# Kernel optimization log

Measured on AMD Instinct MI355X. Metric: run time of the kernel, lower is better.

## Reference

```python
import jax, jax.numpy as jnp
import numpy as np

EMBED_DIM = 256
MIN_SCALE = 0.5
BASE = 100.0
NDIM = 3
EPS = 1e-5


def basis_norm(psi, w):
    # w: [B, N] float weights; reduce over token dim (-2)
    norm_sq = jnp.sum(w[..., None] * (psi * psi), axis=-2, keepdims=True)
    return psi / jnp.sqrt(norm_sq + EPS)


def rotary(f, coords, lift):
    # lift: [D//2, 3]; phase: [B, N, D//2]
    phase = coords @ lift.T
    c, s = jnp.cos(phase), jnp.sin(phase)
    f1, f2 = jnp.split(f, 2, axis=-1)
    return jnp.concatenate([f1 * c - f2 * s, f1 * s + f2 * c], axis=-1)


def setup_inputs() -> dict:
    key = jax.random.key(0)
    ks = jax.random.split(key, 12)
    B, N, D = 4, 8192, EMBED_DIM
    phi = jax.random.normal(ks[0], (B, N, D), dtype=jnp.float32)
    coords = jax.random.normal(ks[1], (B, N, NDIM), dtype=jnp.float32)
    weights = jax.random.uniform(ks[2], (B, N), dtype=jnp.float32)
    scale = 1.0 / np.sqrt(D)
    Wq = jax.random.normal(ks[3], (D, D), dtype=jnp.float32) * scale
    bq = jnp.zeros((D,), dtype=jnp.float32)
    Wk = jax.random.normal(ks[4], (D, D), dtype=jnp.float32) * scale
    bk = jax.random.normal(ks[5], (D,), dtype=jnp.float32) * 0.01
    Wv = jax.random.normal(ks[6], (D, D), dtype=jnp.float32) * scale
    bv = jax.random.normal(ks[7], (D,), dtype=jnp.float32) * 0.01
    Wo = jax.random.normal(ks[8], (D, D), dtype=jnp.float32) * scale
    bo = jnp.zeros((D,), dtype=jnp.float32)
    # rotary lift init: k_norms * random unit vecs
    half = D // 2
    scales = BASE ** (-2.0 * np.arange(half) / D)
    k_norms = (2.0 * np.pi / MIN_SCALE) * scales  # [half]
    u = np.asarray(jax.random.normal(ks[9], (half, NDIM)))
    u = u / np.linalg.norm(u, axis=-1, keepdims=True)
    lift = jnp.asarray(k_norms[:, None] * u, dtype=jnp.float32)  # [half, 3]
    return {"phi": phi, "coords": coords, "weights": weights,
            "Wq": Wq, "bq": bq, "Wk": Wk, "bk": bk, "Wv": Wv, "bv": bv,
            "Wo": Wo, "bo": bo, "lift": lift}


def reference(phi, coords, weights, Wq, bq, Wk, bk, Wv, bv, Wo, bo, lift):
    q = phi @ Wq.T + bq
    k = basis_norm(phi @ Wk.T + bk, weights)
    v = basis_norm(phi @ Wv.T + bv, weights)
    q = rotary(q, coords, lift)
    k = rotary(k, coords, lift)
    k = k * weights[..., None]  # float-weights branch
    kv = jnp.einsum('bnd,bne->bde', k, v)   # [B, D, D]
    out = jnp.einsum('bnd,bde->bne', q, kv)  # [B, N, D]
    return out @ Wo.T + bo
```

## Files before the change

### kernel.cpp

```cpp
#include <hip/hip_runtime.h>
#include <hip/hip_bf16.h>
#include <stdint.h>

#define DEV __device__ __forceinline__

typedef short short8 __attribute__((ext_vector_type(8)));
typedef float floatx4 __attribute__((ext_vector_type(4)));

constexpr int D = 256;
constexpr int NTOK = 8192;
constexpr int MTOT = 4 * NTOK;

DEV void gl_lds16(const void* g, void* l) {
  __builtin_amdgcn_global_load_lds(
      (const __attribute__((address_space(1))) void*)g,
      (__attribute__((address_space(3))) void*)l, 16, 0, 0);
}

DEV float bflo(uint32_t u) { return __uint_as_float(u << 16); }
DEV float bfhi(uint32_t u) { return __uint_as_float(u & 0xffff0000u); }
DEV uint32_t packbf(float a, float b) {
  uint16_t xa = __builtin_bit_cast(uint16_t, __float2bfloat16(a));
  uint16_t xb = __builtin_bit_cast(uint16_t, __float2bfloat16(b));
  return (uint32_t)xa | ((uint32_t)xb << 16);
}

constexpr int PHI_E = MTOT * D;
constexpr int W_E = D * D;
__global__ __launch_bounds__(256) void convert(
    const float* __restrict__ phi, const float* __restrict__ Wq,
    const float* __restrict__ Wk, const float* __restrict__ Wv,
    const float* __restrict__ Wo,
    uint32_t* __restrict__ dst, float2* __restrict__ nszero) {
  if (blockIdx.x == 0) {
    const float2 z = {0.f, 0.f};
#pragma unroll
    for (int k = 0; k < 4; k++) nszero[k * 256 + threadIdx.x] = z;
  }
  const int idx2 = blockIdx.x * 256 + threadIdx.x;
  const int e0 = idx2 * 2;
  float2 v;
  if (e0 < PHI_E) {
    v = ((const float2*)phi)[idx2];
  } else {
    int r = e0 - PHI_E;
    if (r < W_E) v = ((const float2*)Wq)[r >> 1];
    else if (r < 2 * W_E) v = ((const float2*)Wk)[(r - W_E) >> 1];
    else if (r < 3 * W_E) v = ((const float2*)Wv)[(r - 2 * W_E) >> 1];
    else v = ((const float2*)Wo)[(r - 3 * W_E) >> 1];
  }
  dst[idx2] = packbf(v.x, v.y);
}

__global__ __launch_bounds__(256, 2) void gemm_qkv(
    const __hip_bfloat16* __restrict__ phi,
    const __hip_bfloat16* __restrict__ W16,
    const float* __restrict__ bq, const float* __restrict__ bk, const float* __restrict__ bv,
    const float* __restrict__ coords, const float* __restrict__ wts,
    const float* __restrict__ lift,
    __hip_bfloat16* __restrict__ Qb, __hip_bfloat16* __restrict__ Kb,
    __hip_bfloat16* __restrict__ Vb, float* __restrict__ nsk, float* __restrict__ nsv) {
  __shared__ __align__(16) char As[8192];
  __shared__ __align__(16) char Bs[16384];
  const int t = threadIdx.x, lane = t & 63, wid = t >> 6;
  const int wm = (wid & 1) * 64, wn = (wid >> 1) * 64;
  const int l16 = lane & 15, q4 = lane >> 4;
  const int bid = blockIdx.x;
  const int g = (bid & 7) * 96 + (bid >> 3);
  const int mat = g % 3;
  const int m0 = (g / 3) * 128;
  const __hip_bfloat16* W = W16 + (size_t)mat * W_E;
  const float* bias = (mat == 0) ? bq : (mat == 1) ? bk : bv;
  __hip_bfloat16* Out = (mat == 0) ? Qb : (mat == 1) ? Kb : Vb;

  floatx4 acc[4][8] = {};

  const int srow = wid * 16 + (lane >> 2);
  const int skoff = (lane & 3) * 8;
  const __hip_bfloat16* gA = phi + (size_t)(m0 + srow) * D + skoff;
  const __hip_bfloat16* gB = W + (size_t)srow * D + skoff;
  char* lA = As + srow * 64 + skoff * 2;
  char* lB = Bs + srow * 64 + skoff * 2;

  for (int kt = 0; kt < 256; kt += 32) {
    gl_lds16(gA + kt, lA);
    gl_lds16(gA + kt + 64 * D, lA + 4096);
    gl_lds16(gB + kt, lB);
    gl_lds16(gB + kt + 64 * D, lB + 4096);
    gl_lds16(gB + kt + 128 * D, lB + 8192);
    gl_lds16(gB + kt + 192 * D, lB + 12288);
    __syncthreads();
    short8 af[4], bf8[8];
#pragma unroll
    for (int i = 0; i < 4; i++)
      af[i] = *(const short8*)(As + (wm + i * 16 + l16) * 64 + q4 * 16);
#pragma unroll
    for (int j = 0; j < 8; j++) {
      const int col = wn + (j & 3) * 16 + (j >> 2) * 128 + l16;
      bf8[j] = *(const short8*)(Bs + col * 64 + q4 * 16);
    }
#pragma unroll
    for (int i = 0; i < 4; i++)
#pragma unroll
      for (int j = 0; j < 8; j++)
        acc[i][j] = __builtin_amdgcn_mfma_f32_16x16x32_bf16(af[i], bf8[j], acc[i][j], 0, 0, 0);
    __syncthreads();
  }

  float bcol[8];
#pragma unroll
  for (int j = 0; j < 8; j++)
    bcol[j] = bias[wn + (j & 3) * 16 + (j >> 2) * 128 + l16];

  if (mat == 0) {
    float lx[4], ly[4], lz[4];
#pragma unroll
    for (int jj = 0; jj < 4; jj++) {
      const int c = wn + jj * 16 + l16;
      lx[jj] = lift[c * 3 + 0]; ly[jj] = lift[c * 3 + 1]; lz[jj] = lift[c * 3 + 2];
    }
#pragma unroll
    for (int i = 0; i < 4; i++) {
#pragma unroll
      for (int r = 0; r < 4; r++) {
        const int row = m0 + wm + i * 16 + q4 * 4 + r;
        const float cx = coords[row * 3 + 0];
        const float cy = coords[row * 3 + 1];
        const float cz = coords[row * 3 + 2];
#pragma unroll
        for (int jj = 0; jj < 4; jj++) {
          const int c = wn + jj * 16 + l16;
          const float p = cx * lx[jj] + cy * ly[jj] + cz * lz[jj];
          float s, cs;
          __sincosf(p, &s, &cs);
          const float f1 = acc[i][jj][r] + bcol[jj];
          const float f2 = acc[i][jj + 4][r] + bcol[jj + 4];
          Out[(size_t)row * D + c]       = __float2bfloat16(f1 * cs - f2 * s);
          Out[(size_t)row * D + c + 128] = __float2bfloat16(f1 * s + f2 * cs);
        }
      }
    }
  } else {
    const int b = m0 >> 13;
    float* ns = (mat == 1) ? nsk : nsv;
    float colsum[8] = {};
#pragma unroll
    for (int i = 0; i < 4; i++) {
#pragma unroll
      for (int r = 0; r < 4; r++) {
        const int row = m0 + wm + i * 16 + q4 * 4 + r;
        const float w = wts[row];
#pragma unroll
        for (int j = 0; j < 8; j++) {
          const int col = wn + (j & 3) * 16 + (j >> 2) * 128 + l16;
          const float psi = acc[i][j][r] + bcol[j];
          Out[(size_t)row * D + col] = __float2bfloat16(psi);
          colsum[j] += w * psi * psi;
        }
      }
    }
#pragma unroll
    for (int j = 0; j < 8; j++) {
      float s = colsum[j];
      s += __shfl_xor(s, 16);
      s += __shfl_xor(s, 32);
      if (q4 == 0) {
        const int col = wn + (j & 3) * 16 + (j >> 2) * 128 + l16;
        atomicAdd(&ns[b * D + col], s);
      }
    }
  }
}

__global__ __launch_bounds__(256) void kpoint(
    __hip_bfloat16* __restrict__ Kb, const float* __restrict__ coords,
    const float* __restrict__ wts, const float* __restrict__ lift,
    const float* __restrict__ nsk) {
  const int t = threadIdx.x;
  const int j = t & 63, rloc = t >> 6;
  const int r0 = blockIdx.x * 128;
  const int b = r0 >> 13;
  const int j0 = 2 * j, j1 = 2 * j + 1;
  const float lx0 = lift[j0 * 3 + 0], ly0 = lift[j0 * 3 + 1], lz0 = lift[j0 * 3 + 2];
  const float lx1 = lift[j1 * 3 + 0], ly1 = lift[j1 * 3 + 1], lz1 = lift[j1 * 3 + 2];
  const int nb = b * D;
  const float ik0 = rsqrtf(nsk[nb + j0] + 1e-5f);
  const float ik1 = rsqrtf(nsk[nb + j1] + 1e-5f);
  const float ik2 = rsqrtf(nsk[nb + 128 + j0] + 1e-5f);
  const float ik3 = rsqrtf(nsk[nb + 128 + j1] + 1e-5f);
  uint32_t* K32 = (uint32_t*)Kb;
  for (int it = 0; it < 32; it++) {
    const size_t row = (size_t)r0 + it * 4 + rloc;
    const float cx = coords[row * 3 + 0];
    const float cy = coords[row * 3 + 1];
    const float cz = coords[row * 3 + 2];
    const float p0 = cx * lx0 + cy * ly0 + cz * lz0;
    const float p1 = cx * lx1 + cy * ly1 + cz * lz1;
    float s0, c0, s1, c1;
    __sincosf(p0, &s0, &c0);
    __sincosf(p1, &s1, &c1);
    const float w = wts[row];
    const size_t base = row * 128;
    const uint32_t klo = K32[base + j], khi = K32[base + 64 + j];
    const float k1a = bflo(klo) * ik0, k1b = bfhi(klo) * ik1;
    const float k2a = bflo(khi) * ik2, k2b = bfhi(khi) * ik3;
    K32[base + j]      = packbf((k1a * c0 - k2a * s0) * w, (k1b * c1 - k2b * s1) * w);
    K32[base + 64 + j] = packbf((k1a * s0 + k2a * c0) * w, (k1b * s1 + k2b * c1) * w);
  }
}

__global__ __launch_bounds__(256, 2) void gemm_tn(
    const __hip_bfloat16* __restrict__ Kwb, const __hip_bfloat16* __restrict__ Vb,
    __hip_bfloat16* __restrict__ part) {
  __shared__ __align__(16) char Asm[128 * 80];
  __shared__ __align__(16) char Bsm[128 * 80];
  const int t = threadIdx.x, lane = t & 63, wid = t >> 6;
  const int wm = (wid & 1) * 64, wn = (wid >> 1) * 64;
  const int l16 = lane & 15, q4 = lane >> 4;
  const int bid = blockIdx.x;
  const int g = (bid & 7) * 64 + (bid >> 3);
  const int ed = g & 3, rest = g >> 2;
  const int chunk = rest & 31, b = rest >> 5;
  const int e0 = (ed & 1) * 128, d0 = (ed >> 1) * 128;
  const uint32_t* A32 = (const uint32_t*)Kwb;
  const uint32_t* B32 = (const uint32_t*)Vb;
  const int s_np = (((t & 3) | ((t >> 6) << 2)) ^ ((t >> 4) & 3));
  const int s_e2lo = (t >> 2) & 15;
  floatx4 acc[4][4] = {};
  for (int nt = 0; nt < 256; nt += 32) {
    const int nbase = chunk * 256 + nt;
    const size_t tokbase = ((size_t)b * NTOK + nbase + 2 * s_np) * 128;
#pragma unroll
    for (int r = 0; r < 4; r++) {
      const int e2 = s_e2lo + r * 16;
      {
        const uint32_t a0 = A32[tokbase + (d0 >> 1) + e2];
        const uint32_t a1 = A32[tokbase + 128 + (d0 >> 1) + e2];
        *(uint32_t*)(Asm + (2 * e2) * 80 + 4 * s_np)     = (a0 & 0xffffu) | (a1 << 16);
        *(uint32_t*)(Asm + (2 * e2 + 1) * 80 + 4 * s_np) = (a0 >> 16) | (a1 & 0xffff0000u);
      }
      {
        const uint32_t b0 = B32[tokbase + (e0 >> 1) + e2];
        const uint32_t b1 = B32[tokbase + 128 + (e0 >> 1) + e2];
        *(uint32_t*)(Bsm + (2 * e2) * 80 + 4 * s_np)     = (b0 & 0xffffu) | (b1 << 16);
        *(uint32_t*)(Bsm + (2 * e2 + 1) * 80 + 4 * s_np) = (b0 >> 16) | (b1 & 0xffff0000u);
      }
    }
    __syncthreads();
    short8 af[4], bf8[4];
#pragma unroll
    for (int i = 0; i < 4; i++) {
      af[i]  = *(const short8*)(Asm + (wm + i * 16 + l16) * 80 + q4 * 16);
      bf8[i] = *(const short8*)(Bsm + (wn + i * 16 + l16) * 80 + q4 * 16);
    }
#pragma unroll
    for (int i = 0; i < 4; i++)
#pragma unroll
      for (int j = 0; j < 4; j++)
        acc[i][j] = __builtin_amdgcn_mfma_f32_16x16x32_bf16(af[i], bf8[j], acc[i][j], 0, 0, 0);
    __syncthreads();
  }
  __hip_bfloat16* pt = part + (((size_t)(chunk * 4 + b)) << 16);
#pragma unroll
  for (int i = 0; i < 4; i++) {
#pragma unroll
    for (int r = 0; r < 4; r++) {
      const int rg = d0 + wm + i * 16 + q4 * 4 + r;
#pragma unroll
      for (int j = 0; j < 4; j++) {
        const int cg = e0 + wn + j * 16 + l16;
        pt[rg * 256 + cg] = __float2bfloat16(acc[i][j][r]);
      }
    }
  }
}

__global__ __launch_bounds__(256) void reduce_kvt(const uint32_t* __restrict__ part,
                                                  uint32_t* __restrict__ Ps,
                                                  const float* __restrict__ nsv) {
  const int flat2 = blockIdx.x * 256 + threadIdx.x;
  const int b = flat2 >> 15;
  const int off = flat2 & 32767;
  const int es = (off & 127) * 2;
  float sx = 0, sy = 0;
#pragma unroll
  for (int c = 0; c < 32; c++) {
    const uint32_t u = part[(((size_t)(c * 4 + b)) << 15) + off];
    sx += bflo(u); sy += bfhi(u);
  }
  const float iv0 = rsqrtf(nsv[b * D + es] + 1e-5f);
  const float iv1 = rsqrtf(nsv[b * D + es + 1] + 1e-5f);
  Ps[flat2] = packbf(sx * iv0, sy * iv1);
}

__global__ __launch_bounds__(256, 2) void gemm_mt(
    const __hip_bfloat16* __restrict__ Wo16, const __hip_bfloat16* __restrict__ Ps,
    __hip_bfloat16* __restrict__ MT) {
  __shared__ __align__(16) char As[8192];
  __shared__ __align__(16) char Bs[8192];
  const int t = threadIdx.x, lane = t & 63, wid = t >> 6;
  const int wm = (wid & 1) * 64, wn = (wid >> 1) * 64;
  const int l16 = lane & 15, q4 = lane >> 4;
  const int m0 = blockIdx.x * 128, n0 = blockIdx.y * 128, b = blockIdx.z;
  const __hip_bfloat16* Bm = Ps + ((size_t)b << 16);
  floatx4 acc[4][4] = {};
  const int srow = wid * 16 + (lane >> 2);
  const int skoff = (lane & 3) * 8;
  const __hip_bfloat16* gA = Wo16 + (size_t)(m0 + srow) * D + skoff;
  const __hip_bfloat16* gB = Bm + (size_t)(n0 + srow) * D + skoff;
  char* lA = As + srow * 64 + skoff * 2;
  char* lB = Bs + srow * 64 + skoff * 2;
  for (int kt = 0; kt < 256; kt += 32) {
    gl_lds16(gA + kt, lA);
    gl_lds16(gA + kt + 64 * D, lA + 4096);
    gl_lds16(gB + kt, lB);
    gl_lds16(gB + kt + 64 * D, lB + 4096);
    __syncthreads();
    short8 af[4], bf8[4];
#pragma unroll
    for (int i = 0; i < 4; i++) {
      af[i]  = *(const short8*)(As + (wm + i * 16 + l16) * 64 + q4 * 16);
      bf8[i] = *(const short8*)(Bs + (wn + i * 16 + l16) * 64 + q4 * 16);
    }
#pragma unroll
    for (int i = 0; i < 4; i++)
#pragma unroll
      for (int j = 0; j < 4; j++)
        acc[i][j] = __builtin_amdgcn_mfma_f32_16x16x32_bf16(af[i], bf8[j], acc[i][j], 0, 0, 0);
    __syncthreads();
  }
  __hip_bfloat16* Ob = MT + ((size_t)b << 16);
#pragma unroll
  for (int j = 0; j < 4; j++) {
    const int colg = n0 + wn + j * 16 + l16;
#pragma unroll
    for (int i = 0; i < 4; i++) {
      const int rowg = m0 + wm + i * 16 + q4 * 4;
#pragma unroll
      for (int r = 0; r < 4; r++)
        Ob[(size_t)(rowg + r) * D + colg] = __float2bfloat16(acc[i][j][r]);
    }
  }
}

__global__ __launch_bounds__(256, 2) void gemm_out(
    const __hip_bfloat16* __restrict__ A, const __hip_bfloat16* __restrict__ Pm,
    const float* __restrict__ bo, float* __restrict__ Og) {
  __shared__ __align__(16) char As[8192];
  __shared__ __align__(16) char Bs[8192];
  const int t = threadIdx.x, lane = t & 63, wid = t >> 6;
  const int wm = (wid & 1) * 64, wn = (wid >> 1) * 64;
  const int l16 = lane & 15, q4 = lane >> 4;
  const int m0 = blockIdx.x * 128, n0 = blockIdx.y * 128;
  const int b = m0 >> 13;
  const __hip_bfloat16* W = Pm + ((size_t)b << 16);
  floatx4 acc[4][4] = {};
  const int srow = wid * 16 + (lane >> 2);
  const int skoff = (lane & 3) * 8;
  const __hip_bfloat16* gA = A + (size_t)(m0 + srow) * D + skoff;
  const __hip_bfloat16* gB = W + (size_t)(n0 + srow) * D + skoff;
  char* lA = As + srow * 64 + skoff * 2;
  char* lB = Bs + srow * 64 + skoff * 2;
  for (int kt = 0; kt < 256; kt += 32) {
    gl_lds16(gA + kt, lA);
    gl_lds16(gA + kt + 64 * D, lA + 4096);
    gl_lds16(gB + kt, lB);
    gl_lds16(gB + kt + 64 * D, lB + 4096);
    __syncthreads();
    short8 af[4], bf8[4];
#pragma unroll
    for (int i = 0; i < 4; i++) {
      af[i]  = *(const short8*)(As + (wm + i * 16 + l16) * 64 + q4 * 16);
      bf8[i] = *(const short8*)(Bs + (wn + i * 16 + l16) * 64 + q4 * 16);
    }
#pragma unroll
    for (int i = 0; i < 4; i++)
#pragma unroll
      for (int j = 0; j < 4; j++)
        acc[i][j] = __builtin_amdgcn_mfma_f32_16x16x32_bf16(af[i], bf8[j], acc[i][j], 0, 0, 0);
    __syncthreads();
  }
#pragma unroll
  for (int j = 0; j < 4; j++) {
    const int colg = n0 + wn + j * 16 + l16;
    const float bb = bo[colg];
#pragma unroll
    for (int i = 0; i < 4; i++) {
      const int rowg = m0 + wm + i * 16 + q4 * 4;
#pragma unroll
      for (int r = 0; r < 4; r++)
        Og[(size_t)(rowg + r) * D + colg] = acc[i][j][r] + bb;
    }
  }
}

extern "C" void kernel_launch(void* const* d_in, const int* in_sizes, int n_in,
                              void* d_out, int out_size, void* d_ws, size_t ws_size,
                              hipStream_t stream) {
  const float* phi    = (const float*)d_in[0];
  const float* coords = (const float*)d_in[1];
  const float* wts    = (const float*)d_in[2];
  const float* bq     = (const float*)d_in[4];
  const float* bk     = (const float*)d_in[6];
  const float* bv     = (const float*)d_in[8];
  const float* Wo     = (const float*)d_in[9];
  const float* bo     = (const float*)d_in[10];
  const float* lift   = (const float*)d_in[11];

  char* ws = (char*)d_ws;
  __hip_bfloat16* phi16 = (__hip_bfloat16*)ws;
  __hip_bfloat16* W16   = (__hip_bfloat16*)(ws + 16777216);
  const size_t QOFF = 17301504;
  const size_t SZ = (size_t)MTOT * D * 2;
  __hip_bfloat16* Qb = (__hip_bfloat16*)(ws + QOFF);
  __hip_bfloat16* Kb = (__hip_bfloat16*)(ws + QOFF + SZ);
  __hip_bfloat16* Vb = (__hip_bfloat16*)(ws + QOFF + 2 * SZ);
  const size_t NOFF = QOFF + 3 * SZ;
  float* nsk = (float*)(ws + NOFF);
  float* nsv = (float*)(ws + NOFF + 4096);
  __hip_bfloat16* part = (__hip_bfloat16*)(ws + NOFF + 8192);
  __hip_bfloat16* Ps   = (__hip_bfloat16*)(ws + NOFF + 8192 + 16777216);
  __hip_bfloat16* MT   = (__hip_bfloat16*)(ws + NOFF + 8192 + 16777216 + 524288);

  convert<<<16896, 256, 0, stream>>>(phi, (const float*)d_in[3], (const float*)d_in[5],
                                     (const float*)d_in[7], Wo,
                                     (uint32_t*)ws, (float2*)(ws + NOFF));
  gemm_qkv<<<768, 256, 0, stream>>>(phi16, W16, bq, bk, bv, coords, wts, lift,
                                    Qb, Kb, Vb, nsk, nsv);
  kpoint<<<256, 256, 0, stream>>>(Kb, coords, wts, lift, nsk);
  gemm_tn<<<512, 256, 0, stream>>>(Kb, Vb, part);
  reduce_kvt<<<512, 256, 0, stream>>>((const uint32_t*)part, (uint32_t*)Ps, nsv);
  gemm_mt<<<dim3(2, 2, 4), 256, 0, stream>>>(W16 + 3 * W_E, Ps, MT);
  gemm_out<<<dim3(256, 2), 256, 0, stream>>>(Qb, MT, bo, (float*)d_out);
}
```

Measured before the change: 180.9 us.

## Store K and V transposed (feature-major) so KV GEMM uses direct LDS loads

The QKV GEMM epilogue now writes K and V in a transposed [B, D, N] layout with packed 8-byte stores. The rotary/weight kernel is rewritten to walk that layout, one feature pair per block. The K^T V GEMM then loads tiles with global_load_lds instead of the manual transpose-and-repack through padded LDS, and uses 512-token chunks, which halves the number of partials to reduce. The cost is scattered strided writes in the QKV epilogue and fewer blocks (256) in the KV GEMM, which lowers parallelism.

```diff
diff --git a/kernel.cpp b/kernel.cpp
--- a/kernel.cpp
+++ b/kernel.cpp
@@ -71,7 +71,6 @@
   const int m0 = (g / 3) * 128;
   const __hip_bfloat16* W = W16 + (size_t)mat * W_E;
   const float* bias = (mat == 0) ? bq : (mat == 1) ? bk : bv;
-  __hip_bfloat16* Out = (mat == 0) ? Qb : (mat == 1) ? Kb : Vb;
 
   floatx4 acc[4][8] = {};
 
@@ -135,28 +134,40 @@
           __sincosf(p, &s, &cs);
           const float f1 = acc[i][jj][r] + bcol[jj];
           const float f2 = acc[i][jj + 4][r] + bcol[jj + 4];
-          Out[(size_t)row * D + c]       = __float2bfloat16(f1 * cs - f2 * s);
-          Out[(size_t)row * D + c + 128] = __float2bfloat16(f1 * s + f2 * cs);
+          Qb[(size_t)row * D + c]       = __float2bfloat16(f1 * cs - f2 * s);
+          Qb[(size_t)row * D + c + 128] = __float2bfloat16(f1 * s + f2 * cs);
         }
       }
     }
   } else {
     const int b = m0 >> 13;
+    const int tloc = (m0 & 8191) + wm;
     float* ns = (mat == 1) ? nsk : nsv;
+    uint32_t* T32 = (uint32_t*)((mat == 1) ? Kb : Vb);
     float colsum[8] = {};
 #pragma unroll
     for (int i = 0; i < 4; i++) {
+      float w4[4];
+      float psi[8][4];
 #pragma unroll
       for (int r = 0; r < 4; r++) {
         const int row = m0 + wm + i * 16 + q4 * 4 + r;
-        const float w = wts[row];
+        w4[r] = wts[row];
 #pragma unroll
         for (int j = 0; j < 8; j++) {
-          const int col = wn + (j & 3) * 16 + (j >> 2) * 128 + l16;
-          const float psi = acc[i][j][r] + bcol[j];
-          Out[(size_t)row * D + col] = __float2bfloat16(psi);
-          colsum[j] += w * psi * psi;
+          const float p = acc[i][j][r] + bcol[j];
+          psi[j][r] = p;
+          colsum[j] += w4[r] * p * p;
         }
+      }
+      const int tl = tloc + i * 16 + q4 * 4;
+#pragma unroll
+      for (int j = 0; j < 8; j++) {
+        const int col = wn + (j & 3) * 16 + (j >> 2) * 128 + l16;
+        uint2 pk;
+        pk.x = packbf(psi[j][0], psi[j][1]);
+        pk.y = packbf(psi[j][2], psi[j][3]);
+        *(uint2*)&T32[(((size_t)b * 256 + col) << 12) + (tl >> 1)] = pk;
       }
     }
 #pragma unroll
@@ -173,85 +184,66 @@
 }
 
 __global__ __launch_bounds__(256) void kpoint(
-    __hip_bfloat16* __restrict__ Kb, const float* __restrict__ coords,
+    uint32_t* __restrict__ KT32, const float* __restrict__ coords,
     const float* __restrict__ wts, const float* __restrict__ lift,
     const float* __restrict__ nsk) {
+  const int c = blockIdx.x, b = blockIdx.z;
+  const int tok0 = blockIdx.y * 2048;
+  const float lx = lift[c * 3 + 0], ly = lift[c * 3 + 1], lz = lift[c * 3 + 2];
+  const float ik0 = rsqrtf(nsk[b * D + c] + 1e-5f);
+  const float ik1 = rsqrtf(nsk[b * D + c + 128] + 1e-5f);
+  const size_t rlo = ((size_t)b * 256 + c) << 12;
+  const size_t rhi = rlo + ((size_t)128 << 12);
   const int t = threadIdx.x;
-  const int j = t & 63, rloc = t >> 6;
-  const int r0 = blockIdx.x * 128;
-  const int b = r0 >> 13;
-  const int j0 = 2 * j, j1 = 2 * j + 1;
-  const float lx0 = lift[j0 * 3 + 0], ly0 = lift[j0 * 3 + 1], lz0 = lift[j0 * 3 + 2];
-  const float lx1 = lift[j1 * 3 + 0], ly1 = lift[j1 * 3 + 1], lz1 = lift[j1 * 3 + 2];
-  const int nb = b * D;
-  const float ik0 = rsqrtf(nsk[nb + j0] + 1e-5f);
-  const float ik1 = rsqrtf(nsk[nb + j1] + 1e-5f);
-  const float ik2 = rsqrtf(nsk[nb + 128 + j0] + 1e-5f);
-  const float ik3 = rsqrtf(nsk[nb + 128 + j1] + 1e-5f);
-  uint32_t* K32 = (uint32_t*)Kb;
-  for (int it = 0; it < 32; it++) {
-    const size_t row = (size_t)r0 + it * 4 + rloc;
-    const float cx = coords[row * 3 + 0];
-    const float cy = coords[row * 3 + 1];
-    const float cz = coords[row * 3 + 2];
-    const float p0 = cx * lx0 + cy * ly0 + cz * lz0;
-    const float p1 = cx * lx1 + cy * ly1 + cz * lz1;
-    float s0, c0, s1, c1;
-    __sincosf(p0, &s0, &c0);
-    __sincosf(p1, &s1, &c1);
-    const float w = wts[row];
-    const size_t base = row * 128;
-    const uint32_t klo = K32[base + j], khi = K32[base + 64 + j];
-    const float k1a = bflo(klo) * ik0, k1b = bfhi(klo) * ik1;
-    const float k2a = bflo(khi) * ik2, k2b = bfhi(khi) * ik3;
-    K32[base + j]      = packbf((k1a * c0 - k2a * s0) * w, (k1b * c1 - k2b * s1) * w);
-    K32[base + 64 + j] = packbf((k1a * s0 + k2a * c0) * w, (k1b * s1 + k2b * c1) * w);
+#pragma unroll
+  for (int it = 0; it < 4; it++) {
+    const int dw = (tok0 >> 1) + it * 256 + t;
+    const size_t gtok = (size_t)b * NTOK + dw * 2;
+    const float cx0 = coords[gtok * 3 + 0], cy0 = coords[gtok * 3 + 1], cz0 = coords[gtok * 3 + 2];
+    const float cx1 = coords[gtok * 3 + 3], cy1 = coords[gtok * 3 + 4], cz1 = coords[gtok * 3 + 5];
+    float s0, co0, s1, co1;
+    __sincosf(cx0 * lx + cy0 * ly + cz0 * lz, &s0, &co0);
+    __sincosf(cx1 * lx + cy1 * ly + cz1 * lz, &s1, &co1);
+    const float w0 = wts[gtok], w1 = wts[gtok + 1];
+    const uint32_t lo = KT32[rlo + dw], hi = KT32[rhi + dw];
+    const float f1e = bflo(lo) * ik0, f1o = bfhi(lo) * ik0;
+    const float f2e = bflo(hi) * ik1, f2o = bfhi(hi) * ik1;
+    KT32[rlo + dw] = packbf((f1e * co0 - f2e * s0) * w0, (f1o * co1 - f2o * s1) * w1);
+    KT32[rhi + dw] = packbf((f1e * s0 + f2e * co0) * w0, (f1o * s1 + f2o * co1) * w1);
   }
 }
 
 __global__ __launch_bounds__(256, 2) void gemm_tn(
-    const __hip_bfloat16* __restrict__ Kwb, const __hip_bfloat16* __restrict__ Vb,
+    const __hip_bfloat16* __restrict__ KT, const __hip_bfloat16* __restrict__ VT,
     __hip_bfloat16* __restrict__ part) {
-  __shared__ __align__(16) char Asm[128 * 80];
-  __shared__ __align__(16) char Bsm[128 * 80];
+  __shared__ __align__(16) char As[8192];
+  __shared__ __align__(16) char Bs[8192];
   const int t = threadIdx.x, lane = t & 63, wid = t >> 6;
   const int wm = (wid & 1) * 64, wn = (wid >> 1) * 64;
   const int l16 = lane & 15, q4 = lane >> 4;
   const int bid = blockIdx.x;
-  const int g = (bid & 7) * 64 + (bid >> 3);
-  const int ed = g & 3, rest = g >> 2;
-  const int chunk = rest & 31, b = rest >> 5;
-  const int e0 = (ed & 1) * 128, d0 = (ed >> 1) * 128;
-  const uint32_t* A32 = (const uint32_t*)Kwb;
-  const uint32_t* B32 = (const uint32_t*)Vb;
-  const int s_np = (((t & 3) | ((t >> 6) << 2)) ^ ((t >> 4) & 3));
-  const int s_e2lo = (t >> 2) & 15;
+  const int g = (bid & 7) * 32 + (bid >> 3);
+  const int ed = g & 3, chunk = (g >> 2) & 15, b = g >> 6;
+  const int d0 = (ed >> 1) * 128, e0 = (ed & 1) * 128;
+  const int srow = wid * 16 + (lane >> 2);
+  const int skoff = (lane & 3) * 8;
+  const int tokb = chunk * 512;
+  const __hip_bfloat16* gA = KT + (((size_t)b * 256 + d0 + srow) << 13) + tokb + skoff;
+  const __hip_bfloat16* gB = VT + (((size_t)b * 256 + e0 + srow) << 13) + tokb + skoff;
+  char* lA = As + srow * 64 + skoff * 2;
+  char* lB = Bs + srow * 64 + skoff * 2;
   floatx4 acc[4][4] = {};
-  for (int nt = 0; nt < 256; nt += 32) {
-    const int nbase = chunk * 256 + nt;
-    const size_t tokbase = ((size_t)b * NTOK + nbase + 2 * s_np) * 128;
-#pragma unroll
-    for (int r = 0; r < 4; r++) {
-      const int e2 = s_e2lo + r * 16;
-      {
-        const uint32_t a0 = A32[tokbase + (d0 >> 1) + e2];
-        const uint32_t a1 = A32[tokbase + 128 + (d0 >> 1) + e2];
-        *(uint32_t*)(Asm + (2 * e2) * 80 + 4 * s_np)     = (a0 & 0xffffu) | (a1 << 16);
-        *(uint32_t*)(Asm + (2 * e2 + 1) * 80 + 4 * s_np) = (a0 >> 16) | (a1 & 0xffff0000u);
-      }
-      {
-        const uint32_t b0 = B32[tokbase + (e0 >> 1) + e2];
-        const uint32_t b1 = B32[tokbase + 128 + (e0 >> 1) + e2];
-        *(uint32_t*)(Bsm + (2 * e2) * 80 + 4 * s_np)     = (b0 & 0xffffu) | (b1 << 16);
-        *(uint32_t*)(Bsm + (2 * e2 + 1) * 80 + 4 * s_np) = (b0 >> 16) | (b1 & 0xffff0000u);
-      }
-    }
+  for (int kt = 0; kt < 512; kt += 32) {
+    gl_lds16(gA + kt, lA);
+    gl_lds16(gA + kt + ((size_t)64 << 13), lA + 4096);
+    gl_lds16(gB + kt, lB);
+    gl_lds16(gB + kt + ((size_t)64 << 13), lB + 4096);
     __syncthreads();
     short8 af[4], bf8[4];
 #pragma unroll
     for (int i = 0; i < 4; i++) {
-      af[i]  = *(const short8*)(Asm + (wm + i * 16 + l16) * 80 + q4 * 16);
-      bf8[i] = *(const short8*)(Bsm + (wn + i * 16 + l16) * 80 + q4 * 16);
+      af[i]  = *(const short8*)(As + (wm + i * 16 + l16) * 64 + q4 * 16);
+      bf8[i] = *(const short8*)(Bs + (wn + i * 16 + l16) * 64 + q4 * 16);
     }
 #pragma unroll
     for (int i = 0; i < 4; i++)
@@ -262,15 +254,14 @@
   }
   __hip_bfloat16* pt = part + (((size_t)(chunk * 4 + b)) << 16);
 #pragma unroll
-  for (int i = 0; i < 4; i++) {
-#pragma unroll
-    for (int r = 0; r < 4; r++) {
-      const int rg = d0 + wm + i * 16 + q4 * 4 + r;
-#pragma unroll
-      for (int j = 0; j < 4; j++) {
-        const int cg = e0 + wn + j * 16 + l16;
-        pt[rg * 256 + cg] = __float2bfloat16(acc[i][j][r]);
-      }
+  for (int j = 0; j < 4; j++) {
+    const int cg = e0 + wn + j * 16 + l16;
+#pragma unroll
+    for (int i = 0; i < 4; i++) {
+      const int rg = d0 + wm + i * 16 + q4 * 4;
+#pragma unroll
+      for (int r = 0; r < 4; r++)
+        pt[(rg + r) * 256 + cg] = __float2bfloat16(acc[i][j][r]);
     }
   }
 }
@@ -284,7 +275,7 @@
   const int es = (off & 127) * 2;
   float sx = 0, sy = 0;
 #pragma unroll
-  for (int c = 0; c < 32; c++) {
+  for (int c = 0; c < 16; c++) {
     const uint32_t u = part[(((size_t)(c * 4 + b)) << 15) + off];
     sx += bflo(u); sy += bfhi(u);
   }
@@ -427,8 +418,8 @@
                                      (uint32_t*)ws, (float2*)(ws + NOFF));
   gemm_qkv<<<768, 256, 0, stream>>>(phi16, W16, bq, bk, bv, coords, wts, lift,
                                     Qb, Kb, Vb, nsk, nsv);
-  kpoint<<<256, 256, 0, stream>>>(Kb, coords, wts, lift, nsk);
-  gemm_tn<<<512, 256, 0, stream>>>(Kb, Vb, part);
+  kpoint<<<dim3(128, 4, 4), 256, 0, stream>>>((uint32_t*)Kb, coords, wts, lift, nsk);
+  gemm_tn<<<256, 256, 0, stream>>>(Kb, Vb, part);
   reduce_kvt<<<512, 256, 0, stream>>>((const uint32_t*)part, (uint32_t*)Ps, nsv);
   gemm_mt<<<dim3(2, 2, 4), 256, 0, stream>>>(W16 + 3 * W_E, Ps, MT);
   gemm_out<<<dim3(256, 2), 256, 0, stream>>>(Qb, MT, bo, (float*)d_out);
```

Result: slower. 190.1 us (+5.1%).
